# Performance work log

Measured on AMD Instinct MI355X. Metric: run time of the kernel, lower is better.

The kernel has to match this reference:

```python
import jax, jax.numpy as jnp
import numpy as np

EMBED_DIM = 1024
N_HEADS = 16
HEAD_DIM = EMBED_DIM // N_HEADS


def setup_inputs() -> dict:
    key = jax.random.key(0)
    ks = jax.random.split(key, 5)
    B, T, C = 4, 2048, EMBED_DIM
    s = 0.02
    return {
        "x": jax.random.normal(ks[0], (B, T, C), dtype=jnp.float32),
        "w_qkv": jax.random.normal(ks[1], (C, 3 * C), dtype=jnp.float32) * s,
        "b_qkv": jnp.zeros((3 * C,), dtype=jnp.float32),
        "w_proj": jax.random.normal(ks[2], (C, C), dtype=jnp.float32) * s,
        "b_proj": jnp.zeros((C,), dtype=jnp.float32),
    }


def reference(x, w_qkv, b_qkv, w_proj, b_proj):
    B, T, C = x.shape
    H, D = N_HEADS, HEAD_DIM
    qkv = x @ w_qkv + b_qkv  # [B,T,3C]
    q, k, v = jnp.split(qkv, 3, axis=-1)
    # [B,H,T,D]
    q = q.reshape(B, T, H, D).transpose(0, 2, 1, 3)
    k = k.reshape(B, T, H, D).transpose(0, 2, 1, 3)
    v = v.reshape(B, T, H, D).transpose(0, 2, 1, 3)
    scale = jnp.asarray(D, x.dtype) ** -0.5
    att = jnp.einsum("bhqd,bhkd->bhqk", q, k) * scale  # [B,H,T,T]
    causal = jnp.tril(jnp.ones((T, T), dtype=bool))
    att = jnp.where(causal, att, jnp.asarray(-jnp.inf, att.dtype))
    att = jax.nn.softmax(att, axis=-1)
    out = jnp.einsum("bhqk,bhkd->bhqd", att, v)  # [B,H,T,D]
    out = out.transpose(0, 2, 1, 3).reshape(B, T, C)
    return out @ w_proj + b_proj
```

## Files before the change

kernel.cpp:

```cpp
#include <hip/hip_runtime.h>
#include <hip/hip_bf16.h>


typedef __bf16 bf16x8 __attribute__((ext_vector_type(8)));
typedef float f32x4 __attribute__((ext_vector_type(4)));
typedef unsigned short u16x8 __attribute__((ext_vector_type(8)));
typedef unsigned short u16x4 __attribute__((ext_vector_type(4)));
typedef unsigned int u32;

#define LOG2E 1.44269504088896340736f
#define NEG_INF (-__builtin_inff())

#define AS_GLOBAL(p) ((const __attribute__((address_space(1))) u32*)(p))
#define AS_LDS(p) ((__attribute__((address_space(3))) u32*)(p))

__device__ __forceinline__ unsigned short f2bf(float f) {
  unsigned int u = __builtin_bit_cast(unsigned int, f);
  u += 0x7fff + ((u >> 16) & 1);
  return (unsigned short)(u >> 16);
}

__device__ __forceinline__ u32 cvt_pk_bf16(float lo, float hi) {
  u32 r;
  asm("v_cvt_pk_bf16_f32 %0, %1, %2" : "=v"(r) : "v"(lo), "v"(hi));
  return r;
}

__device__ __forceinline__ bf16x8 ld_frag(const unsigned short* p) {
  return __builtin_bit_cast(bf16x8, *reinterpret_cast<const u16x8*>(p));
}

__global__ void k_convert(const float* __restrict__ in, unsigned short* __restrict__ out, int n4) {
  int i = blockIdx.x * blockDim.x + threadIdx.x;
  int stride = gridDim.x * blockDim.x;
  for (; i < n4; i += stride) {
    float4 v = reinterpret_cast<const float4*>(in)[i];
    u16x4 o = { f2bf(v.x), f2bf(v.y), f2bf(v.z), f2bf(v.w) };
    reinterpret_cast<u16x4*>(out)[i] = o;
  }
}

__global__ void k_transpose(const float* __restrict__ in, unsigned short* __restrict__ out,
                            int K, int N, int scaleN, float scl,
                            const float* __restrict__ bias_in, float* __restrict__ bias_out) {
  __shared__ float tile[32][33];
  int n0 = blockIdx.x * 32, k0 = blockIdx.y * 32;
  int tx = threadIdx.x & 31, ty = threadIdx.x >> 5;
#pragma unroll
  for (int i = 0; i < 4; i++)
    tile[ty + i * 8][tx] = in[(size_t)(k0 + ty + i * 8) * N + n0 + tx];
  if (bias_out && k0 == 0 && ty == 0) {
    int n = n0 + tx;
    bias_out[n] = bias_in[n] * (n < scaleN ? scl : 1.f);
  }
  __syncthreads();
#pragma unroll
  for (int i = 0; i < 4; i++) {
    int n = n0 + ty + i * 8;
    float v = tile[tx][ty + i * 8];
    if (n < scaleN) v *= scl;
    out[(size_t)n * K + k0 + tx] = f2bf(v);
  }
}

template <bool BF16_OUT>
__global__ __launch_bounds__(256) void k_gemm(
    const unsigned short* __restrict__ A, const unsigned short* __restrict__ Bt,
    const float* __restrict__ bias, void* __restrict__ Cv, int M, int N, int K) {
  constexpr int BK = 64;
  __shared__ unsigned short Asm[128][BK];
  __shared__ unsigned short Bsm[128][BK];
  const int tid = threadIdx.x;
  const int lane = tid & 63, w = tid >> 6;
  const int wr = w >> 1, wc = w & 1;
  const int brow = blockIdx.x * 128, bcol = blockIdx.y * 128;
  const int r0 = lane & 15, kq = lane >> 4;

  f32x4 acc[4][4] = {};

  const int srow = lane >> 3;
  const int scol = ((lane & 7) ^ srow) * 8;
  const int swa = (r0 & 7) << 3;

  for (int k0 = 0; k0 < K; k0 += BK) {
    __syncthreads();
#pragma unroll
    for (int q2 = 0; q2 < 4; q2++) {
      int c = w * 4 + q2;
      const unsigned short* ga = &A[(size_t)(brow + c * 8 + srow) * K + k0 + scol];
      const unsigned short* gb = &Bt[(size_t)(bcol + c * 8 + srow) * K + k0 + scol];
      __builtin_amdgcn_global_load_lds(AS_GLOBAL(ga), AS_LDS(&Asm[c * 8][0]), 16, 0, 0);
      __builtin_amdgcn_global_load_lds(AS_GLOBAL(gb), AS_LDS(&Bsm[c * 8][0]), 16, 0, 0);
    }
    __syncthreads();
#pragma unroll
    for (int c = 0; c < 2; c++) {
      bf16x8 af[4], bfr[4];
#pragma unroll
      for (int m = 0; m < 4; m++)
        af[m] = ld_frag(&Asm[wr * 64 + m * 16 + r0][(c * 32 + kq * 8) ^ swa]);
#pragma unroll
      for (int n = 0; n < 4; n++)
        bfr[n] = ld_frag(&Bsm[wc * 64 + n * 16 + r0][(c * 32 + kq * 8) ^ swa]);
      __builtin_amdgcn_s_setprio(1);
#pragma unroll
      for (int m = 0; m < 4; m++)
#pragma unroll
        for (int n = 0; n < 4; n++)
          acc[m][n] = __builtin_amdgcn_mfma_f32_16x16x32_bf16(af[m], bfr[n], acc[m][n], 0, 0, 0);
      __builtin_amdgcn_s_setprio(0);
    }
  }

  const int orow = kq * 4;
#pragma unroll
  for (int n = 0; n < 4; n++) {
#pragma unroll
    for (int m = 0; m < 4; m++) {
      int col = bcol + wc * 64 + n * 16 + r0;
      float bv = bias[col];
#pragma unroll
      for (int r = 0; r < 4; r++) {
        int row = brow + wr * 64 + m * 16 + orow + r;
        float v = acc[m][n][r] + bv;
        if (BF16_OUT)
          ((unsigned short*)Cv)[(size_t)row * N + col] = f2bf(v);
        else
          ((float*)Cv)[(size_t)row * N + col] = v;
      }
    }
  }
}

__global__ __launch_bounds__(256, 3) void k_flash(const unsigned short* __restrict__ qkv,
                                                  unsigned short* __restrict__ att, int T) {
  constexpr int C3 = 3072, C = 1024;
  __shared__ unsigned short Ksm[2][64][72];
  __shared__ unsigned short Vsm[2][64][72];

  const int tid = threadIdx.x, lane = tid & 63, w = tid >> 6;
  const int bh = blockIdx.x;
  const int qtp = gridDim.y - 1 - blockIdx.y;
  const int b = bh >> 4, h = bh & 15;
  const int q0 = qtp * 128;
  const int r0 = lane & 15, kq = lane >> 4;

  const size_t rowbase = (size_t)b * T * C3;
  const int qb0 = q0 + w * 32, qb1 = qb0 + 16;

  bf16x8 qf[2][2];
  {
    const unsigned short* qp0 = &qkv[rowbase + (size_t)(qb0 + r0) * C3 + h * 64];
    qf[0][0] = ld_frag(&qp0[kq * 8]);
    qf[0][1] = ld_frag(&qp0[32 + kq * 8]);
    const unsigned short* qp1 = qp0 + (size_t)16 * C3;
    qf[1][0] = ld_frag(&qp1[kq * 8]);
    qf[1][1] = ld_frag(&qp1[32 + kq * 8]);
  }

  u16x8 ones_w;
#pragma unroll
  for (int i = 0; i < 8; i++) ones_w[i] = 0x3F80;
  const bf16x8 ones8 = __builtin_bit_cast(bf16x8, ones_w);

  f32x4 accO[2][4] = {};
  f32x4 accl[2] = {{0.f,0.f,0.f,0.f},{0.f,0.f,0.f,0.f}};

  const int stk = tid >> 3, sd8 = (tid & 7) * 8;
  constexpr size_t PSTRIDE = (size_t)32 * C3;
  constexpr size_t TSTRIDE = (size_t)64 * C3;
  const unsigned short* kp0 = &qkv[rowbase + (size_t)stk * C3 + h * 64 + sd8 + C];
  const unsigned short* kp1 = kp0 + PSTRIDE;

  u16x8 kreg[2], vreg[2];
  auto LOADT = [&]() {
    kreg[0] = *reinterpret_cast<const u16x8*>(kp0);
    vreg[0] = *reinterpret_cast<const u16x8*>(kp0 + C);
    kreg[1] = *reinterpret_cast<const u16x8*>(kp1);
    vreg[1] = *reinterpret_cast<const u16x8*>(kp1 + C);
    kp0 += TSTRIDE;
    kp1 += TSTRIDE;
  };
  auto WRITET = [&](int buf) {
#pragma unroll
    for (int p = 0; p < 2; p++) {
      int tkk = p * 32 + stk;
      *reinterpret_cast<u16x8*>(&Ksm[buf][tkk][sd8]) = kreg[p];
      int tkx = tkk ^ sd8;
#pragma unroll
      for (int i = 0; i < 8; i++) Vsm[buf][sd8 + i][tkx] = vreg[p][i];
    }
  };

  auto TILE = [&](int buf, int k0) {
    if (k0 > qb1 + 15) return;
    const unsigned short(*Ks)[72] = Ksm[buf];
    const unsigned short(*Vs)[72] = Vsm[buf];

    f32x4 st[2][4];
    __builtin_amdgcn_s_setprio(1);
#pragma unroll
    for (int s = 0; s < 4; s++) {
      bf16x8 kf0 = ld_frag(&Ks[s * 16 + r0][kq * 8]);
      bf16x8 kf1 = ld_frag(&Ks[s * 16 + r0][32 + kq * 8]);
#pragma unroll
      for (int u = 0; u < 2; u++) {
        f32x4 a = {};
        a = __builtin_amdgcn_mfma_f32_16x16x32_bf16(kf0, qf[u][0], a, 0, 0, 0);
        a = __builtin_amdgcn_mfma_f32_16x16x32_bf16(kf1, qf[u][1], a, 0, 0, 0);
        st[u][s] = a;
      }
    }
    __builtin_amdgcn_s_setprio(0);

    u32 pd[2][2][4];
#pragma unroll
    for (int u = 0; u < 2; u++) {
      const int qbu = u ? qb1 : qb0;
      const int qmy = qbu + r0;
      f32x4 sv[4];
      if (k0 + 63 > qbu) {
#pragma unroll
        for (int s = 0; s < 4; s++)
#pragma unroll
          for (int r = 0; r < 4; r++) {
            int kg = k0 + s * 16 + kq * 4 + r;
            sv[s][r] = (kg > qmy) ? NEG_INF : st[u][s][r];
          }
      } else {
#pragma unroll
        for (int s = 0; s < 4; s++) sv[s] = st[u][s];
      }

#pragma unroll
      for (int s = 0; s < 4; s++) {
        f32x4 p = { exp2f(sv[s][0]), exp2f(sv[s][1]), exp2f(sv[s][2]), exp2f(sv[s][3]) };
        sv[s] = p;
      }
      pd[u][0][0] = cvt_pk_bf16(sv[0][0], sv[0][1]);
      pd[u][0][1] = cvt_pk_bf16(sv[0][2], sv[0][3]);
      pd[u][0][2] = cvt_pk_bf16(sv[1][0], sv[1][1]);
      pd[u][0][3] = cvt_pk_bf16(sv[1][2], sv[1][3]);
      pd[u][1][0] = cvt_pk_bf16(sv[2][0], sv[2][1]);
      pd[u][1][1] = cvt_pk_bf16(sv[2][2], sv[2][3]);
      pd[u][1][2] = cvt_pk_bf16(sv[3][0], sv[3][1]);
      pd[u][1][3] = cvt_pk_bf16(sv[3][2], sv[3][3]);
    }

    __builtin_amdgcn_s_setprio(1);
#pragma unroll
    for (int t = 0; t < 2; t++) {
      bf16x8 pa0 = __builtin_bit_cast(bf16x8, *reinterpret_cast<u16x8*>(pd[0][t]));
      bf16x8 pa1 = __builtin_bit_cast(bf16x8, *reinterpret_cast<u16x8*>(pd[1][t]));
      accl[0] = __builtin_amdgcn_mfma_f32_16x16x32_bf16(pa0, ones8, accl[0], 0, 0, 0);
      accl[1] = __builtin_amdgcn_mfma_f32_16x16x32_bf16(pa1, ones8, accl[1], 0, 0, 0);
#pragma unroll
      for (int n = 0; n < 4; n++) {
        int d = n * 16 + r0;
        int swzb = d & 56;
        const u16x4 lo = *reinterpret_cast<const u16x4*>(&Vs[d][(t * 32 + kq * 4) ^ swzb]);
        const u16x4 hi = *reinterpret_cast<const u16x4*>(&Vs[d][(t * 32 + 16 + kq * 4) ^ swzb]);
        u16x8 vbw;
#pragma unroll
        for (int i = 0; i < 4; i++) { vbw[i] = lo[i]; vbw[4 + i] = hi[i]; }
        bf16x8 vb = __builtin_bit_cast(bf16x8, vbw);
        accO[0][n] = __builtin_amdgcn_mfma_f32_16x16x32_bf16(pa0, vb, accO[0][n], 0, 0, 0);
        accO[1][n] = __builtin_amdgcn_mfma_f32_16x16x32_bf16(pa1, vb, accO[1][n], 0, 0, 0);
      }
    }
    __builtin_amdgcn_s_setprio(0);
  };

  int buf = 0;
  LOADT();
  WRITET(0);
  const int nkt = (q0 + 128) >> 6;
  for (int kt = 0; kt < nkt - 1; kt++) {
    __syncthreads();
    LOADT();
    TILE(buf, kt * 64);
    WRITET(buf ^ 1);
    buf ^= 1;
  }
  __syncthreads();
  TILE(buf, (nkt - 1) * 64);

#pragma unroll
  for (int u = 0; u < 2; u++) {
    const int qbu = u ? qb1 : qb0;
    float lr[4];
#pragma unroll
    for (int r = 0; r < 4; r++) lr[r] = 1.f / accl[u][r];
#pragma unroll
    for (int n = 0; n < 4; n++) {
#pragma unroll
      for (int r = 0; r < 4; r++) {
        int qrow = qbu + kq * 4 + r;
        float v = accO[u][n][r] * lr[r];
        att[((size_t)b * T + qrow) * C + h * 64 + n * 16 + r0] = f2bf(v);
      }
    }
  }
}

extern "C" void kernel_launch(void* const* d_in, const int* in_sizes, int n_in,
                              void* d_out, int out_size, void* d_ws, size_t ws_size,
                              hipStream_t stream) {
  const float* x = (const float*)d_in[0];
  const float* w_qkv = (const float*)d_in[1];
  const float* b_qkv = (const float*)d_in[2];
  const float* w_proj = (const float*)d_in[3];
  const float* b_proj = (const float*)d_in[4];

  constexpr int B = 4, T = 2048, C = 1024, C3 = 3072;
  constexpr int M = B * T;
  constexpr float SCL = 0.125f * LOG2E;

  unsigned short* x_bf = (unsigned short*)d_ws;
  unsigned short* wqkvT = x_bf + (size_t)M * C;
  unsigned short* wprojT = wqkvT + (size_t)C3 * C;
  unsigned short* qkv = wprojT + (size_t)C * C;
  unsigned short* att = qkv + (size_t)M * C3;
  float* bias_s = (float*)(att + (size_t)M * C);

  hipLaunchKernelGGL(k_convert, dim3(2048), dim3(256), 0, stream, x, x_bf, M * C / 4);
  hipLaunchKernelGGL(k_transpose, dim3(C3 / 32, C / 32), dim3(256), 0, stream,
                     w_qkv, wqkvT, C, C3, C, SCL, b_qkv, bias_s);
  hipLaunchKernelGGL(k_transpose, dim3(C / 32, C / 32), dim3(256), 0, stream,
                     w_proj, wprojT, C, C, 0, 1.f, (const float*)nullptr, (float*)nullptr);
  hipLaunchKernelGGL((k_gemm<true>), dim3(M / 128, C3 / 128), dim3(256), 0, stream,
                     x_bf, wqkvT, bias_s, (void*)qkv, M, C3, C);
  hipLaunchKernelGGL(k_flash, dim3(64, 16), dim3(256), 0, stream, qkv, att, T);
  hipLaunchKernelGGL((k_gemm<false>), dim3(M / 128, C / 128), dim3(256), 0, stream,
                     att, wprojT, b_proj, d_out, M, C, C);
}
```

Before: 156.7 us.

## Write V transposed from QKV GEMM epilogue and load V fragments directly in flash

The QKV GEMM epilogue now writes the V columns in transposed [B, C, T] layout through an LDS scratch buffer, and writes Q and K into a compact stride-2048 buffer. The flash kernel reads V fragments straight from global memory into registers, which drops the per-tile scalar transposing LDS writes and the V shared-memory buffer. The block-to-(batch-head, q-tile) mapping is also remapped so that concurrent blocks share heads differently. The cost is uncoalesced-ish small global loads of V in the inner loop, which depend on L2 hits, and extra epilogue work in the GEMM.

```diff
diff --git a/kernel.cpp b/kernel.cpp
--- a/kernel.cpp
+++ b/kernel.cpp
@@ -66,7 +66,8 @@
 template <bool BF16_OUT>
 __global__ __launch_bounds__(256) void k_gemm(
     const unsigned short* __restrict__ A, const unsigned short* __restrict__ Bt,
-    const float* __restrict__ bias, void* __restrict__ Cv, int M, int N, int K) {
+    const float* __restrict__ bias, void* __restrict__ Cv,
+    unsigned short* __restrict__ vT, int M, int N, int K, int ldc) {
   constexpr int BK = 64;
   __shared__ unsigned short Asm[128][BK];
   __shared__ unsigned short Bsm[128][BK];
@@ -112,6 +113,38 @@
     }
   }
 
+  if (vT != nullptr && bcol >= 2048) {
+    __syncthreads();
+    unsigned short(*scr)[64] = (w < 2)
+        ? reinterpret_cast<unsigned short(*)[64]>(&Asm[w * 64][0])
+        : reinterpret_cast<unsigned short(*)[64]>(&Bsm[(w - 2) * 64][0]);
+    const int vcb = (bcol - 2048) + wc * 64;
+    const int tb = brow + wr * 64;
+    const int b_ = tb >> 11, t_in = tb & 2047;
+#pragma unroll
+    for (int n = 0; n < 4; n++) {
+      int col = bcol + wc * 64 + n * 16 + r0;
+      float bv = bias[col];
+      int dd = n * 16 + r0;
+#pragma unroll
+      for (int m = 0; m < 4; m++)
+#pragma unroll
+        for (int r = 0; r < 4; r++)
+          scr[dd][m * 16 + kq * 4 + r] = f2bf(acc[m][n][r] + bv);
+    }
+    asm volatile("s_waitcnt lgkmcnt(0)" ::: "memory");
+    __builtin_amdgcn_sched_barrier(0);
+    const int ch = lane & 7, dl = lane >> 3;
+#pragma unroll
+    for (int e = 0; e < 8; e++) {
+      int dd = e * 8 + dl;
+      u16x8 vv = *reinterpret_cast<const u16x8*>(&scr[dd][ch * 8]);
+      *reinterpret_cast<u16x8*>(
+          &vT[((size_t)(b_ * 1024 + vcb + dd)) * 2048 + t_in + ch * 8]) = vv;
+    }
+    return;
+  }
+
   const int orow = kq * 4;
 #pragma unroll
   for (int n = 0; n < 4; n++) {
@@ -124,36 +157,38 @@
         int row = brow + wr * 64 + m * 16 + orow + r;
         float v = acc[m][n][r] + bv;
         if (BF16_OUT)
-          ((unsigned short*)Cv)[(size_t)row * N + col] = f2bf(v);
+          ((unsigned short*)Cv)[(size_t)row * ldc + col] = f2bf(v);
         else
-          ((float*)Cv)[(size_t)row * N + col] = v;
-      }
-    }
-  }
-}
-
-__global__ __launch_bounds__(256, 3) void k_flash(const unsigned short* __restrict__ qkv,
+          ((float*)Cv)[(size_t)row * ldc + col] = v;
+      }
+    }
+  }
+}
+
+__global__ __launch_bounds__(256, 3) void k_flash(const unsigned short* __restrict__ qk,
+                                                  const unsigned short* __restrict__ vT,
                                                   unsigned short* __restrict__ att, int T) {
-  constexpr int C3 = 3072, C = 1024;
+  constexpr int C2 = 2048, C = 1024;
   __shared__ unsigned short Ksm[2][64][72];
-  __shared__ unsigned short Vsm[2][64][72];
 
   const int tid = threadIdx.x, lane = tid & 63, w = tid >> 6;
-  const int bh = blockIdx.x;
-  const int qtp = gridDim.y - 1 - blockIdx.y;
+  const int bid = blockIdx.y * 64 + blockIdx.x;
+  const int idx = bid >> 3;
+  const int bh = ((bid & 7) << 3) | (idx & 7);
+  const int qtp = 15 - (idx >> 3);
   const int b = bh >> 4, h = bh & 15;
   const int q0 = qtp * 128;
   const int r0 = lane & 15, kq = lane >> 4;
 
-  const size_t rowbase = (size_t)b * T * C3;
+  const size_t rowbase = (size_t)b * T * C2;
   const int qb0 = q0 + w * 32, qb1 = qb0 + 16;
 
   bf16x8 qf[2][2];
   {
-    const unsigned short* qp0 = &qkv[rowbase + (size_t)(qb0 + r0) * C3 + h * 64];
+    const unsigned short* qp0 = &qk[rowbase + (size_t)(qb0 + r0) * C2 + h * 64];
     qf[0][0] = ld_frag(&qp0[kq * 8]);
     qf[0][1] = ld_frag(&qp0[32 + kq * 8]);
-    const unsigned short* qp1 = qp0 + (size_t)16 * C3;
+    const unsigned short* qp1 = qp0 + (size_t)16 * C2;
     qf[1][0] = ld_frag(&qp1[kq * 8]);
     qf[1][1] = ld_frag(&qp1[32 + kq * 8]);
   }
@@ -167,35 +202,39 @@
   f32x4 accl[2] = {{0.f,0.f,0.f,0.f},{0.f,0.f,0.f,0.f}};
 
   const int stk = tid >> 3, sd8 = (tid & 7) * 8;
-  constexpr size_t PSTRIDE = (size_t)32 * C3;
-  constexpr size_t TSTRIDE = (size_t)64 * C3;
-  const unsigned short* kp0 = &qkv[rowbase + (size_t)stk * C3 + h * 64 + sd8 + C];
+  constexpr size_t PSTRIDE = (size_t)32 * C2;
+  constexpr size_t TSTRIDE = (size_t)64 * C2;
+  const unsigned short* kp0 = &qk[rowbase + (size_t)stk * C2 + h * 64 + sd8 + C];
   const unsigned short* kp1 = kp0 + PSTRIDE;
 
-  u16x8 kreg[2], vreg[2];
+  const unsigned short* vbase = vT + ((size_t)(b * 1024 + h * 64 + r0)) * 2048 + kq * 4;
+
+  u16x8 kreg[2];
   auto LOADT = [&]() {
     kreg[0] = *reinterpret_cast<const u16x8*>(kp0);
-    vreg[0] = *reinterpret_cast<const u16x8*>(kp0 + C);
     kreg[1] = *reinterpret_cast<const u16x8*>(kp1);
-    vreg[1] = *reinterpret_cast<const u16x8*>(kp1 + C);
     kp0 += TSTRIDE;
     kp1 += TSTRIDE;
   };
   auto WRITET = [&](int buf) {
 #pragma unroll
-    for (int p = 0; p < 2; p++) {
-      int tkk = p * 32 + stk;
-      *reinterpret_cast<u16x8*>(&Ksm[buf][tkk][sd8]) = kreg[p];
-      int tkx = tkk ^ sd8;
-#pragma unroll
-      for (int i = 0; i < 8; i++) Vsm[buf][sd8 + i][tkx] = vreg[p][i];
-    }
+    for (int p = 0; p < 2; p++)
+      *reinterpret_cast<u16x8*>(&Ksm[buf][p * 32 + stk][sd8]) = kreg[p];
   };
 
   auto TILE = [&](int buf, int k0) {
     if (k0 > qb1 + 15) return;
     const unsigned short(*Ks)[72] = Ksm[buf];
-    const unsigned short(*Vs)[72] = Vsm[buf];
+
+    u16x4 vlo[2][4], vhi[2][4];
+#pragma unroll
+    for (int t = 0; t < 2; t++)
+#pragma unroll
+      for (int n = 0; n < 4; n++) {
+        const unsigned short* p = vbase + (size_t)n * (16 * 2048) + k0 + t * 32;
+        vlo[t][n] = *reinterpret_cast<const u16x4*>(p);
+        vhi[t][n] = *reinterpret_cast<const u16x4*>(p + 16);
+      }
 
     f32x4 st[2][4];
     __builtin_amdgcn_s_setprio(1);
@@ -256,13 +295,9 @@
       accl[1] = __builtin_amdgcn_mfma_f32_16x16x32_bf16(pa1, ones8, accl[1], 0, 0, 0);
 #pragma unroll
       for (int n = 0; n < 4; n++) {
-        int d = n * 16 + r0;
-        int swzb = d & 56;
-        const u16x4 lo = *reinterpret_cast<const u16x4*>(&Vs[d][(t * 32 + kq * 4) ^ swzb]);
-        const u16x4 hi = *reinterpret_cast<const u16x4*>(&Vs[d][(t * 32 + 16 + kq * 4) ^ swzb]);
         u16x8 vbw;
 #pragma unroll
-        for (int i = 0; i < 4; i++) { vbw[i] = lo[i]; vbw[4 + i] = hi[i]; }
+        for (int i = 0; i < 4; i++) { vbw[i] = vlo[t][n][i]; vbw[4 + i] = vhi[t][n][i]; }
         bf16x8 vb = __builtin_bit_cast(bf16x8, vbw);
         accO[0][n] = __builtin_amdgcn_mfma_f32_16x16x32_bf16(pa0, vb, accO[0][n], 0, 0, 0);
         accO[1][n] = __builtin_amdgcn_mfma_f32_16x16x32_bf16(pa1, vb, accO[1][n], 0, 0, 0);
@@ -319,8 +354,9 @@
   unsigned short* x_bf = (unsigned short*)d_ws;
   unsigned short* wqkvT = x_bf + (size_t)M * C;
   unsigned short* wprojT = wqkvT + (size_t)C3 * C;
-  unsigned short* qkv = wprojT + (size_t)C * C;
-  unsigned short* att = qkv + (size_t)M * C3;
+  unsigned short* qk2 = wprojT + (size_t)C * C;
+  unsigned short* vTb = qk2 + (size_t)M * 2048;
+  unsigned short* att = vTb + (size_t)B * C * T;
   float* bias_s = (float*)(att + (size_t)M * C);
 
   hipLaunchKernelGGL(k_convert, dim3(2048), dim3(256), 0, stream, x, x_bf, M * C / 4);
@@ -329,8 +365,8 @@
   hipLaunchKernelGGL(k_transpose, dim3(C / 32, C / 32), dim3(256), 0, stream,
                      w_proj, wprojT, C, C, 0, 1.f, (const float*)nullptr, (float*)nullptr);
   hipLaunchKernelGGL((k_gemm<true>), dim3(M / 128, C3 / 128), dim3(256), 0, stream,
-                     x_bf, wqkvT, bias_s, (void*)qkv, M, C3, C);
-  hipLaunchKernelGGL(k_flash, dim3(64, 16), dim3(256), 0, stream, qkv, att, T);
+                     x_bf, wqkvT, bias_s, (void*)qk2, vTb, M, C3, C, 2048);
+  hipLaunchKernelGGL(k_flash, dim3(64, 16), dim3(256), 0, stream, qk2, vTb, att, T);
   hipLaunchKernelGGL((k_gemm<false>), dim3(M / 128, C / 128), dim3(256), 0, stream,
-                     att, wprojT, b_proj, d_out, M, C, C);
-}
+                     att, wprojT, b_proj, d_out, (unsigned short*)nullptr, M, C, C, C);
+}
```

Result: slower. 242.9 us (+55.0%).
